# Kernel optimization log

Measured on AMD Instinct MI355X. Metric: run time of the kernel, lower is better.

## Reference

```python
import jax, jax.numpy as jnp
import numpy as np

N = 8192
D_IN = 512
D_OUT = 512


def setup_inputs() -> dict:
    key = jax.random.key(0)
    k1, k2, k3, k4 = jax.random.split(key, 4)
    x = jax.random.normal(k1, (N, D_IN), dtype=jnp.float32)
    adj = jax.random.uniform(k2, (N, N), dtype=jnp.float32)
    # nn.Linear params: weight (out, in), bias (out,)
    bound = 1.0 / np.sqrt(D_IN)
    W = jax.random.uniform(k3, (D_OUT, D_IN), minval=-bound, maxval=bound, dtype=jnp.float32)
    b = jax.random.uniform(k4, (D_OUT,), minval=-bound, maxval=bound, dtype=jnp.float32)
    return {"x": x, "adj": adj, "W": W, "b": b}


def reference(x, adj, W, b):
    # Symmetric normalization: D^-1/2 (A + I) D^-1/2.
    # Original uses diag-matmuls; broadcast scaling is the identical math
    # without the O(n^3) diagonal GEMMs.
    a = adj + jnp.eye(adj.shape[0], dtype=adj.dtype)
    d = jnp.sum(a, axis=1) ** -0.5  # (N,)
    a_norm = d[:, None] * a * d[None, :]
    support = a_norm @ x                      # (N, D_IN)
    out = support @ W.T + b                   # (N, D_OUT)
    out = jax.nn.relu(out)
    # dropout: identity in eval/reference mode
    return out
```

## Files before the change

### kernel.cpp

```cpp
#include <hip/hip_runtime.h>
#include <stdint.h>

typedef __bf16 bf16_t;
typedef __bf16 bf16x8 __attribute__((ext_vector_type(8)));
typedef __bf16 bf16x4v __attribute__((ext_vector_type(4)));
typedef float f32x16 __attribute__((ext_vector_type(16)));

#define AS_GLOBAL __attribute__((address_space(1)))
#define AS_LDS    __attribute__((address_space(3)))

static constexpr int NN   = 8192;
static constexpr int DIN  = 512;
static constexpr int DOUT = 512;
static constexpr int SPLITK = 2;

__device__ __forceinline__ void async_cp16(const bf16_t* g, bf16_t* l) {
  __builtin_amdgcn_global_load_lds((AS_GLOBAL unsigned int*)g,
                                   (AS_LDS unsigned int*)l, 16, 0, 0);
}

__global__ __launch_bounds__(256) void k_rowsum_convert(
    const float* __restrict__ adj, bf16_t* __restrict__ adjb,
    float* __restrict__ d) {
  const int row = blockIdx.x;
  const int t = threadIdx.x;
  const float4* rf4 = (const float4*)(adj + (size_t)row * NN);
  bf16_t* outp = adjb + (size_t)row * NN;
  const int diagF4 = row >> 2;
  float sum = 0.f;
#pragma unroll
  for (int c = 0; c < 8; ++c) {
    int f4i = c * 256 + t;
    float4 a = rf4[f4i];
    sum += a.x + a.y + a.z + a.w;
    bf16x4v o;
    o[0] = (bf16_t)a.x; o[1] = (bf16_t)a.y; o[2] = (bf16_t)a.z; o[3] = (bf16_t)a.w;
    if (f4i == diagF4) {
      int s = row & 3;
      float vv = s == 0 ? a.x : s == 1 ? a.y : s == 2 ? a.z : a.w;
      o[s] = (bf16_t)(vv + 1.0f);
    }
    *(bf16x4v*)(outp + f4i * 4) = o;
  }
#pragma unroll
  for (int off = 32; off > 0; off >>= 1) sum += __shfl_down(sum, off);
  __shared__ float red[4];
  if ((t & 63) == 0) red[t >> 6] = sum;
  __syncthreads();
  if (t == 0) {
    float s = red[0] + red[1] + red[2] + red[3] + 1.0f;
    d[row] = rsqrtf(s);
  }
}

__global__ __launch_bounds__(256) void k_dx(
    const float* __restrict__ x, const float* __restrict__ d,
    bf16_t* __restrict__ dxb) {
  int idx = blockIdx.x * 256 + threadIdx.x;
  int i = idx >> 7;
  float4 v = *(const float4*)(x + (size_t)idx * 4);
  float s = d[i];
  bf16x4v o;
  o[0] = (bf16_t)(v.x * s); o[1] = (bf16_t)(v.y * s);
  o[2] = (bf16_t)(v.z * s); o[3] = (bf16_t)(v.w * s);
  *(bf16x4v*)(dxb + (size_t)idx * 4) = o;
}

__global__ __launch_bounds__(256) void k_convert_w(
    const float* __restrict__ W, bf16_t* __restrict__ Wb) {
  int idx = blockIdx.x * 256 + threadIdx.x;
  float4 v = *(const float4*)(W + (size_t)idx * 4);
  bf16x4v o;
  o[0] = (bf16_t)v.x; o[1] = (bf16_t)v.y; o[2] = (bf16_t)v.z; o[3] = (bf16_t)v.w;
  *(bf16x4v*)(Wb + (size_t)idx * 4) = o;
}

__device__ __forceinline__ void gemm_tile_128x128_db(
    const bf16_t* __restrict__ A, const bf16_t* __restrict__ B,
    int lda, int ldb, int m0, int n0, int kStart, int kEnd,
    bf16_t* As, bf16_t* Bs, f32x16 acc[2][2]) {
  const int t = threadIdx.x;
  const int lane = t & 63;
  const int wid = t >> 6;
  const int wm = wid >> 1, wn = wid & 1;
  const int l32 = lane & 31, half = lane >> 5;

  const int swz = (t & 7) ^ ((t >> 3) & 7);
  const bf16_t* gA = A + (size_t)(m0 + (t >> 3)) * lda + swz * 8 + kStart;
  const bf16_t* gB = B + (size_t)(n0 + (t >> 3)) * ldb + swz * 8 + kStart;
  const int xorc = lane & 7;
  const int nIter = (kEnd - kStart) >> 6;

#pragma unroll
  for (int i = 0; i < 4; ++i) {
    async_cp16(gA + (size_t)(i * 32) * lda, As + t * 8 + i * 2048);
    async_cp16(gB + (size_t)(i * 32) * ldb, Bs + t * 8 + i * 2048);
  }
  gA += 64; gB += 64;

  int cur = 0;
  for (int it = 0; it < nIter; ++it) {
    if (it + 1 < nIter) {
      const int nb = (cur ^ 1) * 8192;
#pragma unroll
      for (int i = 0; i < 4; ++i) {
        async_cp16(gA + (size_t)(i * 32) * lda, As + nb + t * 8 + i * 2048);
        async_cp16(gB + (size_t)(i * 32) * ldb, Bs + nb + t * 8 + i * 2048);
      }
      gA += 64; gB += 64;
      asm volatile("s_waitcnt vmcnt(8)" ::: "memory");
    } else {
      asm volatile("s_waitcnt vmcnt(0)" ::: "memory");
    }
    __builtin_amdgcn_s_barrier();

    const bf16_t* Ab = As + cur * 8192;
    const bf16_t* Bb = Bs + cur * 8192;
#pragma unroll
    for (int ks = 0; ks < 4; ++ks) {
      const int pchunk = ((ks * 2 + half) ^ xorc) * 8;
      bf16x8 av[2], bv[2];
#pragma unroll
      for (int f = 0; f < 2; ++f) {
        av[f] = *(const bf16x8*)(Ab + (wm * 64 + f * 32 + l32) * 64 + pchunk);
        bv[f] = *(const bf16x8*)(Bb + (wn * 64 + f * 32 + l32) * 64 + pchunk);
      }
#pragma unroll
      for (int fm = 0; fm < 2; ++fm)
#pragma unroll
        for (int fn = 0; fn < 2; ++fn)
          acc[fm][fn] = __builtin_amdgcn_mfma_f32_32x32x16_bf16(
              av[fm], bv[fn], acc[fm][fn], 0, 0, 0);
    }
    asm volatile("s_waitcnt lgkmcnt(0)" ::: "memory");
    __builtin_amdgcn_s_barrier();
    cur ^= 1;
  }
}

__global__ __launch_bounds__(256) void k_gemmY(
    const bf16_t* __restrict__ Wb, const bf16_t* __restrict__ dxb,
    bf16_t* __restrict__ YT) {
  __shared__ __align__(16) bf16_t As[2 * 128 * 64];
  __shared__ __align__(16) bf16_t Bs[2 * 128 * 64];
  f32x16 acc[2][2];
#pragma unroll
  for (int a = 0; a < 2; ++a)
#pragma unroll
    for (int b = 0; b < 2; ++b)
#pragma unroll
      for (int r = 0; r < 16; ++r) acc[a][b][r] = 0.f;

  const int m0 = blockIdx.x * 128, n0 = blockIdx.y * 128;
  gemm_tile_128x128_db(Wb, dxb, DIN, DIN, m0, n0, 0, DIN, As, Bs, acc);

  const int t = threadIdx.x;
  const int lane = t & 63, wid = t >> 6;
  const int wm = wid >> 1, wn = wid & 1;
  const int l32 = lane & 31, half = lane >> 5;
#pragma unroll
  for (int fm = 0; fm < 2; ++fm)
#pragma unroll
    for (int fn = 0; fn < 2; ++fn) {
      int gc = n0 + wn * 64 + fn * 32 + l32;
#pragma unroll
      for (int reg = 0; reg < 16; ++reg) {
        int gr = m0 + wm * 64 + fm * 32 + (reg & 3) + 8 * (reg >> 2) + 4 * half;
        YT[(size_t)gr * NN + gc] = (bf16_t)acc[fm][fn][reg];
      }
    }
}

__global__ __launch_bounds__(256) void k_gemm1(
    const bf16_t* __restrict__ adjb, const bf16_t* __restrict__ YT,
    float* __restrict__ part) {
  __shared__ __align__(16) bf16_t As[2 * 128 * 64];
  __shared__ __align__(16) bf16_t Bs[2 * 128 * 64];
  f32x16 acc[2][2];
#pragma unroll
  for (int a = 0; a < 2; ++a)
#pragma unroll
    for (int b = 0; b < 2; ++b)
#pragma unroll
      for (int r = 0; r < 16; ++r) acc[a][b][r] = 0.f;

  const int m0 = blockIdx.x * 128, n0 = blockIdx.y * 128;
  const int kc = blockIdx.z;
  const int kChunk = NN / SPLITK;
  gemm_tile_128x128_db(adjb, YT, NN, NN, m0, n0, kc * kChunk, (kc + 1) * kChunk,
                       As, Bs, acc);

  const int t = threadIdx.x;
  const int lane = t & 63, wid = t >> 6;
  const int wm = wid >> 1, wn = wid & 1;
  const int l32 = lane & 31, half = lane >> 5;
  float* outp = part + (size_t)kc * NN * DOUT;
#pragma unroll
  for (int fm = 0; fm < 2; ++fm)
#pragma unroll
    for (int fn = 0; fn < 2; ++fn) {
      int gc = n0 + wn * 64 + fn * 32 + l32;
#pragma unroll
      for (int reg = 0; reg < 16; ++reg) {
        int gr = m0 + wm * 64 + fm * 32 + (reg & 3) + 8 * (reg >> 2) + 4 * half;
        outp[(size_t)gr * DOUT + gc] = acc[fm][fn][reg];
      }
    }
}

__global__ __launch_bounds__(256) void k_out(
    const float* __restrict__ part, const float* __restrict__ d,
    const float* __restrict__ bias, float* __restrict__ outp) {
  int idx = blockIdx.x * 256 + threadIdx.x;
  int i = idx >> 7;
  int j4 = idx & 127;
  float4 p = *(const float4*)(part + (size_t)idx * 4);
#pragma unroll
  for (int kc = 1; kc < SPLITK; ++kc) {
    float4 q = *(const float4*)(part + (size_t)kc * NN * DOUT + (size_t)idx * 4);
    p.x += q.x; p.y += q.y; p.z += q.z; p.w += q.w;
  }
  float4 bb = *(const float4*)(bias + j4 * 4);
  float di = d[i];
  float4 o;
  o.x = fmaxf(fmaf(di, p.x, bb.x), 0.f);
  o.y = fmaxf(fmaf(di, p.y, bb.y), 0.f);
  o.z = fmaxf(fmaf(di, p.z, bb.z), 0.f);
  o.w = fmaxf(fmaf(di, p.w, bb.w), 0.f);
  *(float4*)(outp + (size_t)idx * 4) = o;
}

extern "C" void kernel_launch(void* const* d_in, const int* in_sizes, int n_in,
                              void* d_out, int out_size, void* d_ws, size_t ws_size,
                              hipStream_t stream) {
  const float* x   = (const float*)d_in[0];
  const float* adj = (const float*)d_in[1];
  const float* W   = (const float*)d_in[2];
  const float* b   = (const float*)d_in[3];
  float* out = (float*)d_out;

  char* ws = (char*)d_ws;
  bf16_t* adjb = (bf16_t*)(ws);
  float*  part = (float*)(ws + 134217728);
  bf16_t* YT   = (bf16_t*)(ws + 167772160);
  bf16_t* dxb  = (bf16_t*)(ws + 176160768);
  bf16_t* Wb   = (bf16_t*)(ws + 184549376);
  float*  dvec = (float*)(ws + 185073664);

  k_rowsum_convert<<<NN, 256, 0, stream>>>(adj, adjb, dvec);
  k_dx<<<(NN * DIN) / 1024, 256, 0, stream>>>(x, dvec, dxb);
  k_convert_w<<<(DOUT * DIN) / 1024, 256, 0, stream>>>(W, Wb);
  k_gemmY<<<dim3(DOUT / 128, NN / 128), 256, 0, stream>>>(Wb, dxb, YT);
  k_gemm1<<<dim3(NN / 128, DOUT / 128, SPLITK), 256, 0, stream>>>(adjb, YT, part);
  k_out<<<(NN * DOUT) / 1024, 256, 0, stream>>>(part, dvec, b, out);
}
```

Measured before the change: 512.8 us.

## Use 256x256 tiles with 512 threads and split-K 4 in main GEMM; fuse prep kernels

The main adjacency GEMM moves from 128x128 tiles with 256 threads to 256x256 tiles with 512 threads (8 waves, 4x2 MFMA fragments each). Split-K rises to 4 so the grid still fills the GPU, and block indices are remapped so blocks sharing operands run close together. The x-scaling and W-conversion kernels are folded into the row-sum kernel, which saves two launches. The larger tile raises operand reuse and cuts global and LDS traffic per FLOP. In exchange it uses 128KB of LDS per block, needs more registers, and writes twice as much split-K partial data for the final reduction.

```diff
diff --git a/kernel.cpp b/kernel.cpp
--- a/kernel.cpp
+++ b/kernel.cpp
@@ -12,7 +12,7 @@
 static constexpr int NN   = 8192;
 static constexpr int DIN  = 512;
 static constexpr int DOUT = 512;
-static constexpr int SPLITK = 2;
+static constexpr int SPLITK = 4;
 
 __device__ __forceinline__ void async_cp16(const bf16_t* g, bf16_t* l) {
   __builtin_amdgcn_global_load_lds((AS_GLOBAL unsigned int*)g,
@@ -20,7 +20,9 @@
 }
 
 __global__ __launch_bounds__(256) void k_rowsum_convert(
-    const float* __restrict__ adj, bf16_t* __restrict__ adjb,
+    const float* __restrict__ adj, const float* __restrict__ x,
+    const float* __restrict__ W, bf16_t* __restrict__ adjb,
+    bf16_t* __restrict__ dxb, bf16_t* __restrict__ Wb,
     float* __restrict__ d) {
   const int row = blockIdx.x;
   const int t = threadIdx.x;
@@ -47,32 +49,21 @@
   __shared__ float red[4];
   if ((t & 63) == 0) red[t >> 6] = sum;
   __syncthreads();
-  if (t == 0) {
-    float s = red[0] + red[1] + red[2] + red[3] + 1.0f;
-    d[row] = rsqrtf(s);
-  }
-}
-
-__global__ __launch_bounds__(256) void k_dx(
-    const float* __restrict__ x, const float* __restrict__ d,
-    bf16_t* __restrict__ dxb) {
-  int idx = blockIdx.x * 256 + threadIdx.x;
-  int i = idx >> 7;
-  float4 v = *(const float4*)(x + (size_t)idx * 4);
-  float s = d[i];
-  bf16x4v o;
-  o[0] = (bf16_t)(v.x * s); o[1] = (bf16_t)(v.y * s);
-  o[2] = (bf16_t)(v.z * s); o[3] = (bf16_t)(v.w * s);
-  *(bf16x4v*)(dxb + (size_t)idx * 4) = o;
-}
-
-__global__ __launch_bounds__(256) void k_convert_w(
-    const float* __restrict__ W, bf16_t* __restrict__ Wb) {
-  int idx = blockIdx.x * 256 + threadIdx.x;
-  float4 v = *(const float4*)(W + (size_t)idx * 4);
-  bf16x4v o;
-  o[0] = (bf16_t)v.x; o[1] = (bf16_t)v.y; o[2] = (bf16_t)v.z; o[3] = (bf16_t)v.w;
-  *(bf16x4v*)(Wb + (size_t)idx * 4) = o;
+  const float s = rsqrtf(red[0] + red[1] + red[2] + red[3] + 1.0f);
+  if (t == 0) d[row] = s;
+  if (t < 128) {
+    float4 v = *(const float4*)(x + (size_t)row * DIN + t * 4);
+    bf16x4v o;
+    o[0] = (bf16_t)(v.x * s); o[1] = (bf16_t)(v.y * s);
+    o[2] = (bf16_t)(v.z * s); o[3] = (bf16_t)(v.w * s);
+    *(bf16x4v*)(dxb + (size_t)row * DIN + t * 4) = o;
+  } else if (t < 256 && row < DOUT) {
+    int tt = t - 128;
+    float4 v = *(const float4*)(W + (size_t)row * DIN + tt * 4);
+    bf16x4v o;
+    o[0] = (bf16_t)v.x; o[1] = (bf16_t)v.y; o[2] = (bf16_t)v.z; o[3] = (bf16_t)v.w;
+    *(bf16x4v*)(Wb + (size_t)row * DIN + tt * 4) = o;
+  }
 }
 
 __device__ __forceinline__ void gemm_tile_128x128_db(
@@ -171,38 +162,94 @@
     }
 }
 
-__global__ __launch_bounds__(256) void k_gemm1(
+__global__ __launch_bounds__(512, 2) void k_gemm1(
     const bf16_t* __restrict__ adjb, const bf16_t* __restrict__ YT,
     float* __restrict__ part) {
-  __shared__ __align__(16) bf16_t As[2 * 128 * 64];
-  __shared__ __align__(16) bf16_t Bs[2 * 128 * 64];
-  f32x16 acc[2][2];
-#pragma unroll
-  for (int a = 0; a < 2; ++a)
+  __shared__ __align__(16) bf16_t As[2 * 256 * 64];
+  __shared__ __align__(16) bf16_t Bs[2 * 256 * 64];
+  f32x16 acc[4][2];
+#pragma unroll
+  for (int a = 0; a < 4; ++a)
 #pragma unroll
     for (int b = 0; b < 2; ++b)
 #pragma unroll
       for (int r = 0; r < 16; ++r) acc[a][b][r] = 0.f;
 
-  const int m0 = blockIdx.x * 128, n0 = blockIdx.y * 128;
-  const int kc = blockIdx.z;
-  const int kChunk = NN / SPLITK;
-  gemm_tile_128x128_db(adjb, YT, NN, NN, m0, n0, kc * kChunk, (kc + 1) * kChunk,
-                       As, Bs, acc);
+  const int lin = blockIdx.x;
+  const int c = (lin & 7) * 32 + (lin >> 3);
+  const int n0 = (c & 1) * 256;
+  const int m0 = ((c >> 1) & 31) * 256;
+  const int kc = c >> 6;
+  const int kStart = kc * (NN / SPLITK);
+  const int nIter = (NN / SPLITK) >> 6;
 
   const int t = threadIdx.x;
-  const int lane = t & 63, wid = t >> 6;
-  const int wm = wid >> 1, wn = wid & 1;
+  const int lane = t & 63;
+  const int wid = t >> 6;
+  const int wm = wid >> 2, wn = wid & 3;
   const int l32 = lane & 31, half = lane >> 5;
+  const int xorc = lane & 7;
+
+  const int swz = (t & 7) ^ ((t >> 3) & 7);
+  const bf16_t* gA = adjb + (size_t)(m0 + (t >> 3)) * NN + swz * 8 + kStart;
+  const bf16_t* gB = YT   + (size_t)(n0 + (t >> 3)) * NN + swz * 8 + kStart;
+
+#pragma unroll
+  for (int i = 0; i < 4; ++i) {
+    async_cp16(gA + (size_t)(i * 64) * NN, As + t * 8 + i * 4096);
+    async_cp16(gB + (size_t)(i * 64) * NN, Bs + t * 8 + i * 4096);
+  }
+  gA += 64; gB += 64;
+
+  int cur = 0;
+  for (int it = 0; it < nIter; ++it) {
+    if (it + 1 < nIter) {
+      const int nb = (cur ^ 1) * 16384;
+#pragma unroll
+      for (int i = 0; i < 4; ++i) {
+        async_cp16(gA + (size_t)(i * 64) * NN, As + nb + t * 8 + i * 4096);
+        async_cp16(gB + (size_t)(i * 64) * NN, Bs + nb + t * 8 + i * 4096);
+      }
+      gA += 64; gB += 64;
+      asm volatile("s_waitcnt vmcnt(8)" ::: "memory");
+    } else {
+      asm volatile("s_waitcnt vmcnt(0)" ::: "memory");
+    }
+    __builtin_amdgcn_s_barrier();
+
+    const bf16_t* Ab = As + cur * 16384;
+    const bf16_t* Bb = Bs + cur * 16384;
+#pragma unroll
+    for (int ks = 0; ks < 4; ++ks) {
+      const int pchunk = ((ks * 2 + half) ^ xorc) * 8;
+      bf16x8 av[4], bv[2];
+#pragma unroll
+      for (int f = 0; f < 4; ++f)
+        av[f] = *(const bf16x8*)(Ab + (wm * 128 + f * 32 + l32) * 64 + pchunk);
+#pragma unroll
+      for (int f = 0; f < 2; ++f)
+        bv[f] = *(const bf16x8*)(Bb + (wn * 64 + f * 32 + l32) * 64 + pchunk);
+#pragma unroll
+      for (int fm = 0; fm < 4; ++fm)
+#pragma unroll
+        for (int fn = 0; fn < 2; ++fn)
+          acc[fm][fn] = __builtin_amdgcn_mfma_f32_32x32x16_bf16(
+              av[fm], bv[fn], acc[fm][fn], 0, 0, 0);
+    }
+    asm volatile("s_waitcnt lgkmcnt(0)" ::: "memory");
+    __builtin_amdgcn_s_barrier();
+    cur ^= 1;
+  }
+
   float* outp = part + (size_t)kc * NN * DOUT;
 #pragma unroll
-  for (int fm = 0; fm < 2; ++fm)
+  for (int fm = 0; fm < 4; ++fm)
 #pragma unroll
     for (int fn = 0; fn < 2; ++fn) {
       int gc = n0 + wn * 64 + fn * 32 + l32;
 #pragma unroll
       for (int reg = 0; reg < 16; ++reg) {
-        int gr = m0 + wm * 64 + fm * 32 + (reg & 3) + 8 * (reg >> 2) + 4 * half;
+        int gr = m0 + wm * 128 + fm * 32 + (reg & 3) + 8 * (reg >> 2) + 4 * half;
         outp[(size_t)gr * DOUT + gc] = acc[fm][fn][reg];
       }
     }
@@ -242,15 +289,13 @@
   char* ws = (char*)d_ws;
   bf16_t* adjb = (bf16_t*)(ws);
   float*  part = (float*)(ws + 134217728);
-  bf16_t* YT   = (bf16_t*)(ws + 167772160);
-  bf16_t* dxb  = (bf16_t*)(ws + 176160768);
-  bf16_t* Wb   = (bf16_t*)(ws + 184549376);
-  float*  dvec = (float*)(ws + 185073664);
-
-  k_rowsum_convert<<<NN, 256, 0, stream>>>(adj, adjb, dvec);
-  k_dx<<<(NN * DIN) / 1024, 256, 0, stream>>>(x, dvec, dxb);
-  k_convert_w<<<(DOUT * DIN) / 1024, 256, 0, stream>>>(W, Wb);
+  bf16_t* YT   = (bf16_t*)(ws + 201326592);
+  bf16_t* dxb  = (bf16_t*)(ws + 209715200);
+  bf16_t* Wb   = (bf16_t*)(ws + 218103808);
+  float*  dvec = (float*)(ws + 218628096);
+
+  k_rowsum_convert<<<NN, 256, 0, stream>>>(adj, x, W, adjb, dxb, Wb, dvec);
   k_gemmY<<<dim3(DOUT / 128, NN / 128), 256, 0, stream>>>(Wb, dxb, YT);
-  k_gemm1<<<dim3(NN / 128, DOUT / 128, SPLITK), 256, 0, stream>>>(adjb, YT, part);
+  k_gemm1<<<(NN / 256) * (DOUT / 256) * SPLITK, 512, 0, stream>>>(adjb, YT, part);
   k_out<<<(NN * DOUT) / 1024, 256, 0, stream>>>(part, dvec, b, out);
 }
```

Result: no change. 507.9 us (-0.9%).
